# Performance work log

Measured on AMD Instinct MI355X. Metric: run time of the kernel, lower is better.

The kernel has to match this reference:

```python
import jax, jax.numpy as jnp
import numpy as np

N, D, DPE, H = 4096, 256, 16, 8
HD = D // H
SCALE = HD ** -0.5


def setup_inputs() -> dict:
    key = jax.random.key(0)
    ks = jax.random.split(key, 10)
    s = lambda fan_in: 1.0 / np.sqrt(fan_in)
    return {
        "x": jax.random.normal(ks[0], (N, D), jnp.float32),
        "pe": jax.random.normal(ks[1], (N, DPE), jnp.float32),
        "Wqkv": jax.random.uniform(ks[2], (D, 3 * D), jnp.float32, -s(D), s(D)),
        "bqkv": jax.random.uniform(ks[3], (3 * D,), jnp.float32, -s(D), s(D)),
        "Wpe": jax.random.uniform(ks[4], (DPE, H), jnp.float32, -s(DPE), s(DPE)),
        "bpe": jax.random.uniform(ks[5], (H,), jnp.float32, -s(DPE), s(DPE)),
        "Wout": jax.random.uniform(ks[6], (D, D), jnp.float32, -s(D), s(D)),
        "bout": jax.random.uniform(ks[7], (D,), jnp.float32, -s(D), s(D)),
    }


def reference(x, pe, Wqkv, bqkv, Wpe, bpe, Wout, bout):
    # qkv: [N, 3, H, HD] -> q,k,v each [H, N, HD]
    qkv = (x @ Wqkv + bqkv).reshape(N, 3, H, HD).transpose(1, 2, 0, 3)
    q, k, v = qkv[0], qkv[1], qkv[2]
    # attention scores [H, N, N]
    attn = jnp.einsum("hnd,hmd->hnm", q, k) * SCALE
    # pairwise PE-difference bias: bias[h,i,j] = pe_proj[i,h] - pe_proj[j,h]
    pe_proj = pe @ Wpe + bpe  # [N, H]
    pe_bias = (pe_proj[:, None, :] - pe_proj[None, :, :]).transpose(2, 0, 1)
    attn = jax.nn.softmax(attn + pe_bias, axis=-1)
    # dropout disabled (eval mode, p=0)
    out = jnp.einsum("hnm,hmd->nhd", attn, v).reshape(N, D)
    return out @ Wout + bout
```

## Files before the change

### kernel.cpp

```cpp
#include <hip/hip_runtime.h>
#include <math.h>

#define NN 4096
#define HH 8
constexpr float SCALE = 0.17677669529663687f;
constexpr float LOG2E = 1.4426950408889634f;
constexpr float SC2   = SCALE * LOG2E;

typedef __bf16 bf16;
typedef __bf16 bf16x8 __attribute__((ext_vector_type(8)));
typedef __bf16 bf16x4 __attribute__((ext_vector_type(4)));
typedef float  f32x4  __attribute__((ext_vector_type(4)));

#define MFMA(a, b, c) __builtin_amdgcn_mfma_f32_16x16x32_bf16((a), (b), (c), 0, 0, 0)

template <int K, int N, bool SCALEQ>
__device__ __forceinline__ void wcast_body(const float* __restrict__ W,
                                           bf16* __restrict__ WhT,
                                           bf16* __restrict__ WlT,
                                           int n0, int k0, int t,
                                           float (*tile)[65]) {
#pragma unroll
    for (int p = 0; p < 16; ++p) {
        const int r = p * 4 + (t >> 6);
        const int c = t & 63;
        tile[r][c] = W[(size_t)(k0 + r) * N + n0 + c];
    }
    __syncthreads();
    const int nr = t >> 2, kc0 = (t & 3) * 16;
    const float sc = (SCALEQ && (n0 + nr) < 256) ? SC2 : 1.0f;
    bf16x8 h[2], l[2];
#pragma unroll
    for (int g = 0; g < 2; ++g)
#pragma unroll
        for (int j = 0; j < 8; ++j) {
            const float v = tile[kc0 + g * 8 + j][nr] * sc;
            const bf16 hh = (bf16)v;
            h[g][j] = hh;
            l[g][j] = (bf16)(v - (float)hh);
        }
    const size_t ob = (size_t)(n0 + nr) * K + k0 + kc0;
    *(bf16x8*)&WhT[ob] = h[0];
    *(bf16x8*)&WhT[ob + 8] = h[1];
    *(bf16x8*)&WlT[ob] = l[0];
    *(bf16x8*)&WlT[ob + 8] = l[1];
}

__global__ __launch_bounds__(256) void preproc_kernel(
    const float* __restrict__ x, const float* __restrict__ Wqkv,
    const float* __restrict__ Wout, const float* __restrict__ bqkv,
    const float* __restrict__ pe, const float* __restrict__ Wpe,
    const float* __restrict__ bpe,
    bf16* __restrict__ xh, bf16* __restrict__ xl,
    bf16* __restrict__ WqkvhT, bf16* __restrict__ WqkvlT,
    bf16* __restrict__ WouthT, bf16* __restrict__ WoutlT,
    float* __restrict__ bqkv_s, float* __restrict__ ep) {
    __shared__ float tile[64][65];
    const int b = blockIdx.x, t = threadIdx.x;
    if (b < 1024) {
        const int i = (b * 256 + t) * 4;
        const float4 v = *(const float4*)&x[i];
        bf16x4 h, l;
        const float vv[4] = {v.x, v.y, v.z, v.w};
#pragma unroll
        for (int r = 0; r < 4; ++r) {
            h[r] = (bf16)vv[r];
            l[r] = (bf16)(vv[r] - (float)h[r]);
        }
        *(bf16x4*)&xh[i] = h;
        *(bf16x4*)&xl[i] = l;
    } else if (b < 1072) {
        const int bb = b - 1024;
        wcast_body<256, 768, true>(Wqkv, WqkvhT, WqkvlT, (bb % 12) * 64, (bb / 12) * 64, t, tile);
    } else if (b < 1088) {
        const int bb = b - 1072;
        wcast_body<256, 256, false>(Wout, WouthT, WoutlT, (bb % 4) * 64, (bb / 4) * 64, t, tile);
    } else if (b < 1216) {
        const int idx = (b - 1088) * 256 + t;
        const int h = idx >> 12;
        const int n = idx & 4095;
        float acc = bpe[h];
#pragma unroll
        for (int k = 0; k < 16; ++k) acc += pe[n * 16 + k] * Wpe[k * 8 + h];
        ep[h * NN + n] = __builtin_amdgcn_exp2f(-acc * LOG2E - 8.0f);
    } else {
        for (int i = t; i < 768; i += 256)
            bqkv_s[i] = bqkv[i] * (i < 256 ? SC2 : 1.0f);
    }
}

template <int NOUT, int NTILE, typename OT>
__global__ __launch_bounds__(256, 2) void gemm3s_kernel(const bf16* __restrict__ Ah,
                                                        const bf16* __restrict__ Al,
                                                        const bf16* __restrict__ BhT,
                                                        const bf16* __restrict__ BlT,
                                                        const float* __restrict__ bias,
                                                        OT* __restrict__ C) {
    constexpr int NS = NTILE / 16;
    const int t = threadIdx.x, wave = t >> 6, lane = t & 63;
    const int quad = lane >> 4, i16 = lane & 15;
    const int m0 = blockIdx.x * 128 + wave * 32;
    const int n0 = blockIdx.y * NTILE;

    __shared__ __align__(16) bf16 Bs[NTILE * 512];

    {
        const int l = t & 63, i16l = l & 15, ql = l >> 4;
#pragma unroll
        for (int c = t >> 6; c < NS * 16; c += 4) {
            const bool lo = c >= NS * 8;
            const int cc = lo ? c - NS * 8 : c;
            const int nsi = cc >> 3, kc = cc & 7;
            const bf16* src = (lo ? BlT : BhT) +
                (size_t)(n0 + nsi * 16 + i16l) * 256 + kc * 32 + ql * 8;
            *(uint4*)&Bs[c * 512 + l * 8] = *(const uint4*)src;
        }
    }

    bf16x8 ah[2][8], al[2][8];
#pragma unroll
    for (int ms = 0; ms < 2; ++ms) {
        const size_t abase = (size_t)(m0 + ms * 16 + i16) * 256 + quad * 8;
#pragma unroll
        for (int kc = 0; kc < 8; ++kc) {
            ah[ms][kc] = *(const bf16x8*)&Ah[abase + kc * 32];
            al[ms][kc] = *(const bf16x8*)&Al[abase + kc * 32];
        }
    }
    __syncthreads();

#pragma unroll
    for (int nsi = 0; nsi < NS; ++nsi) {
        f32x4 acc[2];
        acc[0] = f32x4{0.f, 0.f, 0.f, 0.f};
        acc[1] = f32x4{0.f, 0.f, 0.f, 0.f};
#pragma unroll
        for (int kc = 0; kc < 8; ++kc) {
            const bf16x8 bh = *(const bf16x8*)&Bs[(nsi * 8 + kc) * 512 + lane * 8];
            const bf16x8 bl = *(const bf16x8*)&Bs[((NS + nsi) * 8 + kc) * 512 + lane * 8];
            acc[0] = MFMA(ah[0][kc], bh, acc[0]);
            acc[0] = MFMA(ah[0][kc], bl, acc[0]);
            acc[0] = MFMA(al[0][kc], bh, acc[0]);
            acc[1] = MFMA(ah[1][kc], bh, acc[1]);
            acc[1] = MFMA(ah[1][kc], bl, acc[1]);
            acc[1] = MFMA(al[1][kc], bh, acc[1]);
        }
        const int n = n0 + nsi * 16 + i16;
        const float b = bias[n];
#pragma unroll
        for (int ms = 0; ms < 2; ++ms)
#pragma unroll
            for (int r = 0; r < 4; ++r)
                C[(size_t)(m0 + ms * 16 + quad * 4 + r) * NOUT + n] = (OT)(acc[ms][r] + b);
    }
}

__global__ __launch_bounds__(256) void kvtrans_kernel(const bf16* __restrict__ qkvb,
                                                      const float* __restrict__ ep,
                                                      bf16* __restrict__ Kf,
                                                      bf16* __restrict__ Vf) {
    const int t = threadIdx.x;
    const int kt = blockIdx.y, h = blockIdx.x;
    __shared__ __align__(16) bf16 Ktile[64 * 32];
    __shared__ __align__(16) bf16 Vtile[64 * 32];
    __shared__ float eps[64];
    {
        const int tok = kt * 64 + (t >> 2);
        const int d8 = (t & 3) * 8;
        *(uint4*)&Ktile[(t >> 2) * 32 + d8] =
            *(const uint4*)&qkvb[(size_t)tok * 768 + 256 + h * 32 + d8];
        *(uint4*)&Vtile[(t >> 2) * 32 + d8] =
            *(const uint4*)&qkvb[(size_t)tok * 768 + 512 + h * 32 + d8];
        if (t < 64) eps[t] = ep[h * NN + kt * 64 + t];
    }
    __syncthreads();
    {
        const int s = t >> 6, l = t & 63, quad = l >> 4, i16 = l & 15;
        bf16x8 o;
#pragma unroll
        for (int j = 0; j < 8; ++j) o[j] = Ktile[(s * 16 + i16) * 32 + quad * 8 + j];
        *(bf16x8*)&Kf[((size_t)(h * 64 + kt) * 4 + s) * 512 + l * 8] = o;
    }
    for (int c = t; c < 384; c += 256) {
        const int ch = c >> 6, ll = c & 63, qd = ll >> 4, ii = ll & 15;
        const int dt = ch >> 1, kc = ch & 1;
        const int dimp = dt * 16 + ii;
        bf16x8 o;
#pragma unroll
        for (int j = 0; j < 8; ++j) {
            const int key = kc * 32 + qd * 8 + j;
            float v;
            if (dimp < 32)       v = (float)Vtile[key * 32 + dimp] * eps[key];
            else if (dimp == 32) v = eps[key];
            else                 v = 0.f;
            o[j] = (bf16)v;
        }
        *(bf16x8*)&Vf[((size_t)(h * 64 + kt) * 6 + ch) * 512 + ll * 8] = o;
    }
}

__global__ __launch_bounds__(256, 2) void attn_kernel(const bf16* __restrict__ qkvb,
                                                      const bf16* __restrict__ Kf,
                                                      const bf16* __restrict__ Vf,
                                                      bf16* __restrict__ aoh,
                                                      bf16* __restrict__ aol) {
    const int t = threadIdx.x, wave = t >> 6, lane = t & 63;
    const int quad = lane >> 4, i16 = lane & 15;
    const int qb = blockIdx.y, h = blockIdx.x;
    const int qg = wave & 1, kh = wave >> 1;

    __shared__ __align__(16) bf16 Pt[4][2][16 * 72];
    __shared__ __align__(16) float Mrg[2][64][24];

    const int q0 = qb * 64 + qg * 32;
    const bf16x8 qf0 = *(const bf16x8*)&qkvb[(size_t)(q0 + i16) * 768 + h * 32 + quad * 8];
    const bf16x8 qf1 = *(const bf16x8*)&qkvb[(size_t)(q0 + 16 + i16) * 768 + h * 32 + quad * 8];

    f32x4 o[3][2];
#pragma unroll
    for (int dt = 0; dt < 3; ++dt)
#pragma unroll
        for (int qs = 0; qs < 2; ++qs) o[dt][qs] = f32x4{0.f, 0.f, 0.f, 0.f};

    const bf16* kb = Kf + (size_t)(h * 64) * 2048 + lane * 8;
    const bf16* vb = Vf + (size_t)(h * 64) * 3072 + lane * 8;
    bf16* ptw = &Pt[wave][0][0];

    const int kt0 = kh * 32;
    bf16x8 kcur[4];
#pragma unroll
    for (int s = 0; s < 4; ++s)
        kcur[s] = *(const bf16x8*)&kb[((size_t)kt0 * 4 + s) * 512];

    for (int it = 0; it < 32; ++it) {
        const int kt = kt0 + it;
        bf16x8 vv[6];
#pragma unroll
        for (int c = 0; c < 6; ++c)
            vv[c] = *(const bf16x8*)&vb[((size_t)kt * 6 + c) * 512];
        bf16x8 knx[4];
        if (it < 31) {
#pragma unroll
            for (int s = 0; s < 4; ++s)
                knx[s] = *(const bf16x8*)&kb[((size_t)(kt + 1) * 4 + s) * 512];
        } else {
#pragma unroll
            for (int s = 0; s < 4; ++s) knx[s] = kcur[s];
        }

        const f32x4 z = {0.f, 0.f, 0.f, 0.f};
        f32x4 sf[4][2];
#pragma unroll
        for (int ks = 0; ks < 4; ++ks) {
            sf[ks][0] = MFMA(kcur[ks], qf0, z);
            sf[ks][1] = MFMA(kcur[ks], qf1, z);
        }

#pragma unroll
        for (int qs = 0; qs < 2; ++qs)
#pragma unroll
            for (int ks = 0; ks < 4; ++ks) {
                bf16x4 pk;
#pragma unroll
                for (int r = 0; r < 4; ++r)
                    pk[r] = (bf16)__builtin_amdgcn_exp2f(sf[ks][qs][r]);
                *(bf16x4*)&ptw[qs * (16 * 72) + i16 * 72 + ks * 16 + quad * 4] = pk;
            }
        asm volatile("s_waitcnt lgkmcnt(0)" ::: "memory");

#pragma unroll
        for (int qs = 0; qs < 2; ++qs) {
            const bf16x8 pb0 = *(const bf16x8*)&ptw[qs * (16 * 72) + i16 * 72 + 0 * 32 + quad * 8];
            const bf16x8 pb1 = *(const bf16x8*)&ptw[qs * (16 * 72) + i16 * 72 + 1 * 32 + quad * 8];
#pragma unroll
            for (int dt = 0; dt < 3; ++dt) {
                o[dt][qs] = MFMA(vv[dt * 2 + 0], pb0, o[dt][qs]);
                o[dt][qs] = MFMA(vv[dt * 2 + 1], pb1, o[dt][qs]);
            }
        }
#pragma unroll
        for (int s = 0; s < 4; ++s) kcur[s] = knx[s];
    }

    if (kh == 1) {
#pragma unroll
        for (int dt = 0; dt < 3; ++dt)
#pragma unroll
            for (int qs = 0; qs < 2; ++qs)
                *(f32x4*)&Mrg[qg][lane][(dt * 2 + qs) * 4] = o[dt][qs];
    }
    __syncthreads();
    if (kh == 0) {
#pragma unroll
        for (int dt = 0; dt < 3; ++dt)
#pragma unroll
            for (int qs = 0; qs < 2; ++qs)
                o[dt][qs] += *(const f32x4*)&Mrg[qg][lane][(dt * 2 + qs) * 4];
        const float linv0 = 1.0f / __shfl(o[2][0][0], i16, 64);
        const float linv1 = 1.0f / __shfl(o[2][1][0], i16, 64);
#pragma unroll
        for (int qs = 0; qs < 2; ++qs) {
            const float inv = qs ? linv1 : linv0;
            const int row = q0 + qs * 16 + i16;
#pragma unroll
            for (int dt = 0; dt < 2; ++dt) {
                bf16x4 hi, lo;
#pragma unroll
                for (int r = 0; r < 4; ++r) {
                    const float v = o[dt][qs][r] * inv;
                    hi[r] = (bf16)v;
                    lo[r] = (bf16)(v - (float)hi[r]);
                }
                const size_t ob = (size_t)row * 256 + h * 32 + dt * 16 + quad * 4;
                *(bf16x4*)&aoh[ob] = hi;
                *(bf16x4*)&aol[ob] = lo;
            }
        }
    }
}

extern "C" void kernel_launch(void* const* d_in, const int* in_sizes, int n_in,
                              void* d_out, int out_size, void* d_ws, size_t ws_size,
                              hipStream_t stream) {
    const float* x    = (const float*)d_in[0];
    const float* pe   = (const float*)d_in[1];
    const float* Wqkv = (const float*)d_in[2];
    const float* bqkv = (const float*)d_in[3];
    const float* Wpe  = (const float*)d_in[4];
    const float* bpe  = (const float*)d_in[5];
    const float* Wout = (const float*)d_in[6];
    const float* bout = (const float*)d_in[7];
    float* out = (float*)d_out;

    char* ws = (char*)d_ws;
    bf16*  xh      = (bf16*)(ws);
    bf16*  xl      = (bf16*)(ws + 2097152);
    bf16*  WqkvhT  = (bf16*)(ws + 4194304);
    bf16*  WqkvlT  = (bf16*)(ws + 4587520);
    bf16*  WouthT  = (bf16*)(ws + 4980736);
    bf16*  WoutlT  = (bf16*)(ws + 5111808);
    float* bqkv_s  = (float*)(ws + 5242880);
    bf16*  qkvb    = (bf16*)(ws + 5245952);
    float* ep      = (float*)(ws + 11537408);
    bf16*  Kf      = (bf16*)(ws + 11668480);
    bf16*  Vf      = (bf16*)(ws + 13765632);
    bf16*  aoh     = (bf16*)(ws + 16911360);
    bf16*  aol     = (bf16*)(ws + 19008512);

    preproc_kernel<<<1217, 256, 0, stream>>>(x, Wqkv, Wout, bqkv, pe, Wpe, bpe,
                                             xh, xl, WqkvhT, WqkvlT, WouthT, WoutlT,
                                             bqkv_s, ep);
    gemm3s_kernel<768, 48, bf16><<<dim3(32, 16), 256, 0, stream>>>(xh, xl, WqkvhT, WqkvlT, bqkv_s, qkvb);
    kvtrans_kernel<<<dim3(HH, 64), 256, 0, stream>>>(qkvb, ep, Kf, Vf);
    attn_kernel<<<dim3(HH, NN / 64), 256, 0, stream>>>(qkvb, Kf, Vf, aoh, aol);
    gemm3s_kernel<256, 16, float><<<dim3(32, 16), 256, 0, stream>>>(aoh, aol, WouthT, WoutlT, bout, out);
}
```

Before: 132.9 us.

## Give each wave all 64 queries and split keys four ways per block

Each of the four waves now handles all 64 query rows of the block over a quarter of the key range, instead of two query groups times two key halves. Every K/V fragment loaded from global memory is reused across 64 queries instead of 32, halving per-block K/V traffic. The cost is more accumulator and Q registers per wave, a larger LDS footprint for P and the merge buffer, and a three-way reduction at the end, which may reduce occupancy under the existing launch bounds.

```diff
diff --git a/kernel.cpp b/kernel.cpp
--- a/kernel.cpp
+++ b/kernel.cpp
@@ -204,42 +204,42 @@
                                                       const bf16* __restrict__ Vf,
                                                       bf16* __restrict__ aoh,
                                                       bf16* __restrict__ aol) {
-    const int t = threadIdx.x, wave = t >> 6, lane = t & 63;
+    const int t = threadIdx.x, kh = t >> 6, lane = t & 63;
     const int quad = lane >> 4, i16 = lane & 15;
     const int qb = blockIdx.y, h = blockIdx.x;
-    const int qg = wave & 1, kh = wave >> 1;
-
-    __shared__ __align__(16) bf16 Pt[4][2][16 * 72];
-    __shared__ __align__(16) float Mrg[2][64][24];
-
-    const int q0 = qb * 64 + qg * 32;
-    const bf16x8 qf0 = *(const bf16x8*)&qkvb[(size_t)(q0 + i16) * 768 + h * 32 + quad * 8];
-    const bf16x8 qf1 = *(const bf16x8*)&qkvb[(size_t)(q0 + 16 + i16) * 768 + h * 32 + quad * 8];
-
-    f32x4 o[3][2];
+
+    __shared__ __align__(16) bf16 Pt[4][4][16 * 72];
+    __shared__ __align__(16) float Mrg[3][64][48];
+
+    const int q0 = qb * 64;
+    bf16x8 qf[4];
+#pragma unroll
+    for (int qs = 0; qs < 4; ++qs)
+        qf[qs] = *(const bf16x8*)&qkvb[(size_t)(q0 + qs * 16 + i16) * 768 + h * 32 + quad * 8];
+
+    f32x4 o[3][4];
 #pragma unroll
     for (int dt = 0; dt < 3; ++dt)
 #pragma unroll
-        for (int qs = 0; qs < 2; ++qs) o[dt][qs] = f32x4{0.f, 0.f, 0.f, 0.f};
+        for (int qs = 0; qs < 4; ++qs) o[dt][qs] = f32x4{0.f, 0.f, 0.f, 0.f};
 
     const bf16* kb = Kf + (size_t)(h * 64) * 2048 + lane * 8;
     const bf16* vb = Vf + (size_t)(h * 64) * 3072 + lane * 8;
-    bf16* ptw = &Pt[wave][0][0];
-
-    const int kt0 = kh * 32;
+
+    const int kt0 = kh * 16;
     bf16x8 kcur[4];
 #pragma unroll
     for (int s = 0; s < 4; ++s)
         kcur[s] = *(const bf16x8*)&kb[((size_t)kt0 * 4 + s) * 512];
 
-    for (int it = 0; it < 32; ++it) {
+    for (int it = 0; it < 16; ++it) {
         const int kt = kt0 + it;
         bf16x8 vv[6];
 #pragma unroll
         for (int c = 0; c < 6; ++c)
             vv[c] = *(const bf16x8*)&vb[((size_t)kt * 6 + c) * 512];
         bf16x8 knx[4];
-        if (it < 31) {
+        if (it < 15) {
 #pragma unroll
             for (int s = 0; s < 4; ++s)
                 knx[s] = *(const bf16x8*)&kb[((size_t)(kt + 1) * 4 + s) * 512];
@@ -249,29 +249,33 @@
         }
 
         const f32x4 z = {0.f, 0.f, 0.f, 0.f};
-        f32x4 sf[4][2];
-#pragma unroll
-        for (int ks = 0; ks < 4; ++ks) {
-            sf[ks][0] = MFMA(kcur[ks], qf0, z);
-            sf[ks][1] = MFMA(kcur[ks], qf1, z);
-        }
-
-#pragma unroll
-        for (int qs = 0; qs < 2; ++qs)
+#pragma unroll
+        for (int qh = 0; qh < 2; ++qh) {
+            f32x4 sf[2][4];
 #pragma unroll
             for (int ks = 0; ks < 4; ++ks) {
-                bf16x4 pk;
-#pragma unroll
-                for (int r = 0; r < 4; ++r)
-                    pk[r] = (bf16)__builtin_amdgcn_exp2f(sf[ks][qs][r]);
-                *(bf16x4*)&ptw[qs * (16 * 72) + i16 * 72 + ks * 16 + quad * 4] = pk;
+                sf[0][ks] = MFMA(kcur[ks], qf[qh * 2 + 0], z);
+                sf[1][ks] = MFMA(kcur[ks], qf[qh * 2 + 1], z);
             }
+#pragma unroll
+            for (int qi = 0; qi < 2; ++qi) {
+                const int qs = qh * 2 + qi;
+#pragma unroll
+                for (int ks = 0; ks < 4; ++ks) {
+                    bf16x4 pk;
+#pragma unroll
+                    for (int r = 0; r < 4; ++r)
+                        pk[r] = (bf16)__builtin_amdgcn_exp2f(sf[qi][ks][r]);
+                    *(bf16x4*)&Pt[kh][qs][i16 * 72 + ks * 16 + quad * 4] = pk;
+                }
+            }
+        }
         asm volatile("s_waitcnt lgkmcnt(0)" ::: "memory");
 
 #pragma unroll
-        for (int qs = 0; qs < 2; ++qs) {
-            const bf16x8 pb0 = *(const bf16x8*)&ptw[qs * (16 * 72) + i16 * 72 + 0 * 32 + quad * 8];
-            const bf16x8 pb1 = *(const bf16x8*)&ptw[qs * (16 * 72) + i16 * 72 + 1 * 32 + quad * 8];
+        for (int qs = 0; qs < 4; ++qs) {
+            const bf16x8 pb0 = *(const bf16x8*)&Pt[kh][qs][i16 * 72 + 0 * 32 + quad * 8];
+            const bf16x8 pb1 = *(const bf16x8*)&Pt[kh][qs][i16 * 72 + 1 * 32 + quad * 8];
 #pragma unroll
             for (int dt = 0; dt < 3; ++dt) {
                 o[dt][qs] = MFMA(vv[dt * 2 + 0], pb0, o[dt][qs]);
@@ -282,32 +286,32 @@
         for (int s = 0; s < 4; ++s) kcur[s] = knx[s];
     }
 
-    if (kh == 1) {
+    if (kh != 0) {
 #pragma unroll
         for (int dt = 0; dt < 3; ++dt)
 #pragma unroll
-            for (int qs = 0; qs < 2; ++qs)
-                *(f32x4*)&Mrg[qg][lane][(dt * 2 + qs) * 4] = o[dt][qs];
+            for (int qs = 0; qs < 4; ++qs)
+                *(f32x4*)&Mrg[kh - 1][lane][(dt * 4 + qs) * 4] = o[dt][qs];
     }
     __syncthreads();
     if (kh == 0) {
 #pragma unroll
-        for (int dt = 0; dt < 3; ++dt)
-#pragma unroll
-            for (int qs = 0; qs < 2; ++qs)
-                o[dt][qs] += *(const f32x4*)&Mrg[qg][lane][(dt * 2 + qs) * 4];
-        const float linv0 = 1.0f / __shfl(o[2][0][0], i16, 64);
-        const float linv1 = 1.0f / __shfl(o[2][1][0], i16, 64);
-#pragma unroll
-        for (int qs = 0; qs < 2; ++qs) {
-            const float inv = qs ? linv1 : linv0;
+        for (int w = 0; w < 3; ++w)
+#pragma unroll
+            for (int dt = 0; dt < 3; ++dt)
+#pragma unroll
+                for (int qs = 0; qs < 4; ++qs)
+                    o[dt][qs] += *(const f32x4*)&Mrg[w][lane][(dt * 4 + qs) * 4];
+#pragma unroll
+        for (int qs = 0; qs < 4; ++qs) {
+            const float linv = 1.0f / __shfl(o[2][qs][0], i16, 64);
             const int row = q0 + qs * 16 + i16;
 #pragma unroll
             for (int dt = 0; dt < 2; ++dt) {
                 bf16x4 hi, lo;
 #pragma unroll
                 for (int r = 0; r < 4; ++r) {
-                    const float v = o[dt][qs][r] * inv;
+                    const float v = o[dt][qs][r] * linv;
                     hi[r] = (bf16)v;
                     lo[r] = (bf16)(v - (float)hi[r]);
                 }
```

After: 130.3 us. 2.0% less time.
